# Performance work log

Hardware: AMD Instinct MI355X
Metric: run time of the kernel (lower is better)

## Reference

```python
import jax, jax.numpy as jnp
import numpy as np

N = 50000       # num entities
F_IN = 256      # input feature dim
H = 128         # hidden_dim (= per-head dim, concat=False)
HEADS = 4
L = 3           # num_layers
T = 3           # num edge types
E = 250000      # edges per type
NEG = 0.2       # leaky_relu slope (module + GATv2 default)


def setup_inputs() -> dict:
    key = jax.random.key(0)
    ks = jax.random.split(key, 10)
    s = 0.05
    return {
        "feat": jax.random.normal(ks[0], (N, F_IN), jnp.float32),
        "emb_table": jax.random.normal(ks[1], (N, H), jnp.float32),
        "proj_w": jax.random.normal(ks[2], (F_IN, H), jnp.float32) * s,
        "proj_b": jnp.zeros((H,), jnp.float32),
        "ln_g": jnp.ones((H,), jnp.float32),
        "ln_b": jnp.zeros((H,), jnp.float32),
        "skip_w": jnp.ones((L,), jnp.float32),
        "Wl": jax.random.normal(ks[3], (L, T, H, HEADS * H), jnp.float32) * s,
        "Wr": jax.random.normal(ks[4], (L, T, H, HEADS * H), jnp.float32) * s,
        "att": jax.random.normal(ks[5], (L, T, HEADS, H), jnp.float32) * s,
        "bias": jnp.zeros((L, T, H), jnp.float32),
        "edge_src": jax.random.randint(ks[6], (T, E), 0, N, jnp.int64),
        "edge_dst": jax.random.randint(ks[7], (T, E), 0, N, jnp.int64),
    }


def _layer_norm(x, g, b):
    mu = jnp.mean(x, axis=-1, keepdims=True)
    var = jnp.mean(jnp.square(x - mu), axis=-1, keepdims=True)
    return (x - mu) * jax.lax.rsqrt(var + 1e-5) * g + b


def _l2norm(x):
    n = jnp.sqrt(jnp.sum(jnp.square(x), axis=-1, keepdims=True))
    return x / jnp.maximum(n, 1e-12)


def _gatv2(x, wl, wr, a, b, src, dst):
    # x: [N,H]; wl,wr: [H, HEADS*H]; a: [HEADS,H]; src/dst: [E]
    xl = (x @ wl).reshape(N, HEADS, H)
    xr = (x @ wr).reshape(N, HEADS, H)
    m = xl[src] + xr[dst]                                   # [E,HEADS,H]
    e = jnp.sum(a * jax.nn.leaky_relu(m, NEG), axis=-1)     # [E,HEADS]
    # segment softmax over incoming edges per destination node
    emax = jax.lax.stop_gradient(jax.ops.segment_max(e, dst, num_segments=N))
    ex = jnp.exp(e - emax[dst])
    den = jax.ops.segment_sum(ex, dst, num_segments=N)      # [N,HEADS]
    alpha = ex / (den[dst] + 1e-16)                         # [E,HEADS]
    out = jax.ops.segment_sum(alpha[:, :, None] * xl[src], dst, num_segments=N)
    return jnp.mean(out, axis=1) + b                        # concat=False -> head mean


def reference(feat, emb_table, proj_w, proj_b, ln_g, ln_b, skip_w,
              Wl, Wr, att, bias, edge_src, edge_dst):
    h = jax.nn.leaky_relu(_layer_norm(feat @ proj_w + proj_b, ln_g, ln_b), NEG)
    ne = _l2norm(emb_table)                                 # normalize(embedding(arange(N)))
    x0 = 0.7 * h + 0.5 * ne
    x = x0
    for i in range(L):
        # HeteroConv(aggr='mean') over edge types, all on node type 'entity'
        per_type = [
            _gatv2(x, Wl[i, t], Wr[i, t], att[i, t], bias[i, t],
                   edge_src[t], edge_dst[t])
            for t in range(T)
        ]
        xu = jnp.mean(jnp.stack(per_type, axis=0), axis=0)
        alpha = jax.nn.sigmoid(skip_w[i])
        x = jax.nn.leaky_relu(xu, NEG) + alpha * x0          # dropout = identity (eval)
    return x
```

## Files before the change

### kernel.cpp

```cpp
#include <hip/hip_runtime.h>
#include <hip/hip_bf16.h>
#include <math.h>

#define N_NODES 50000
#define NOFF    50004
#define NBLK    49
#define F_IN    256
#define H       128
#define HEADS   4
#define HH      512
#define L_LAYERS 3
#define T_TYPES  3
#define E_EDGES  250000
#define NEG      0.2f

typedef __attribute__((ext_vector_type(8))) short short8_t;
typedef __attribute__((ext_vector_type(4))) float float4_t;

__device__ __forceinline__ float leaky(float x) { return x > 0.f ? x : NEG * x; }

__device__ __forceinline__ unsigned short f2bf(float f) {
    union { float f; unsigned int i; } v; v.f = f;
    unsigned int x = v.i;
    unsigned int r = (x + 0x7fffu + ((x >> 16) & 1u)) >> 16;
    return (unsigned short)r;
}

__device__ __forceinline__ float bf2f(unsigned short u) {
    union { unsigned int i; float f; } v; v.i = ((unsigned)u) << 16; return v.f;
}

__device__ __forceinline__ void unpack8(uint4 q, float* o) {
    union { unsigned int i; float f; } v;
    v.i = q.x << 16;          o[0] = v.f;
    v.i = q.x & 0xffff0000u;  o[1] = v.f;
    v.i = q.y << 16;          o[2] = v.f;
    v.i = q.y & 0xffff0000u;  o[3] = v.f;
    v.i = q.z << 16;          o[4] = v.f;
    v.i = q.z & 0xffff0000u;  o[5] = v.f;
    v.i = q.w << 16;          o[6] = v.f;
    v.i = q.w & 0xffff0000u;  o[7] = v.f;
}

__global__ void detect_kernel(const int* __restrict__ edst, int* __restrict__ flag) {
    __shared__ int s_any;
    if (threadIdx.x == 0) s_any = 0;
    __syncthreads();
    int a = 0;
    #pragma unroll
    for (int j = 0; j < 8; ++j) a |= edst[2 * (threadIdx.x * 8 + j) + 1];
    if (a) atomicOr(&s_any, 1);
    __syncthreads();
    if (threadIdx.x == 0) *flag = s_any ? 0 : 1;
}

__global__ void hist_kernel(const int* __restrict__ edst, int* __restrict__ counts,
                            const int* __restrict__ flag) {
    int idx = blockIdx.x * 256 + threadIdx.x;
    if (idx < T_TYPES * E_EDGES) {
        int sh = *flag;
        int t = idx / E_EDGES;
        int d = edst[(size_t)idx << sh];
        if ((unsigned)d < N_NODES)
            atomicAdd(&counts[t * N_NODES + d], 1);
    }
}

__global__ __launch_bounds__(256) void scan_a_kernel(const int* __restrict__ counts,
                                                     int* __restrict__ bsum) {
    const int b = blockIdx.x;
    const int t = b / NBLK, ch = b % NBLK;
    const int tid = threadIdx.x, lane = tid & 63;
    __shared__ int ws[4];
    const int* cnt = counts + t * N_NODES;
    int i0 = ch * 1024 + tid * 4;
    int s = 0;
    if (i0 + 3 < N_NODES) { int4 v = *(const int4*)(cnt + i0); s = v.x + v.y + v.z + v.w; }
    else { for (int j = 0; j < 4; ++j) { int i = i0 + j; if (i < N_NODES) s += cnt[i]; } }
    #pragma unroll
    for (int o = 32; o > 0; o >>= 1) s += __shfl_xor(s, o);
    if (lane == 0) ws[tid >> 6] = s;
    __syncthreads();
    if (tid == 0) bsum[b] = ws[0] + ws[1] + ws[2] + ws[3];
}

__global__ void scan_b_kernel(int* __restrict__ bsum, int* __restrict__ off) {
    int t = threadIdx.x;
    if (t < T_TYPES) {
        int run = 0;
        for (int c = 0; c < NBLK; ++c) { int v = bsum[t * NBLK + c]; bsum[t * NBLK + c] = run; run += v; }
        off[t * NOFF + N_NODES] = run;
    }
}

__global__ __launch_bounds__(256) void scan_c_kernel(const int* counts,
                                                     const int* __restrict__ bsum,
                                                     int* __restrict__ off,
                                                     int* cursor) {
    const int b = blockIdx.x;
    const int t = b / NBLK, ch = b % NBLK;
    const int tid = threadIdx.x, lane = tid & 63, w = tid >> 6;
    __shared__ int ws[4];
    const int* cnt = counts + t * N_NODES;
    int i0 = ch * 1024 + tid * 4;
    int v0 = 0, v1 = 0, v2 = 0, v3 = 0;
    if (i0 + 3 < N_NODES) { int4 v = *(const int4*)(cnt + i0); v0 = v.x; v1 = v.y; v2 = v.z; v3 = v.w; }
    else {
        if (i0     < N_NODES) v0 = cnt[i0];
        if (i0 + 1 < N_NODES) v1 = cnt[i0 + 1];
        if (i0 + 2 < N_NODES) v2 = cnt[i0 + 2];
        if (i0 + 3 < N_NODES) v3 = cnt[i0 + 3];
    }
    int s = v0 + v1 + v2 + v3;
    int x = s;
    #pragma unroll
    for (int o = 1; o < 64; o <<= 1) { int y = __shfl_up(x, o); if (lane >= o) x += y; }
    if (lane == 63) ws[w] = x;
    __syncthreads();
    int woff = 0;
    #pragma unroll
    for (int j = 0; j < 4; ++j) woff += (j < w) ? ws[j] : 0;
    int base = bsum[b] + woff + (x - s);
    int e0 = base, e1 = e0 + v0, e2 = e1 + v1, e3 = e2 + v2;
    if (i0 + 3 < N_NODES) {
        *(int4*)(off + t * NOFF + i0)       = make_int4(e0, e1, e2, e3);
        *(int4*)(cursor + t * N_NODES + i0) = make_int4(e0, e1, e2, e3);
    } else {
        if (i0     < N_NODES) { off[t * NOFF + i0]     = e0; cursor[t * N_NODES + i0]     = e0; }
        if (i0 + 1 < N_NODES) { off[t * NOFF + i0 + 1] = e1; cursor[t * N_NODES + i0 + 1] = e1; }
        if (i0 + 2 < N_NODES) { off[t * NOFF + i0 + 2] = e2; cursor[t * N_NODES + i0 + 2] = e2; }
        if (i0 + 3 < N_NODES) { off[t * NOFF + i0 + 3] = e3; cursor[t * N_NODES + i0 + 3] = e3; }
    }
}

__global__ void scatter_kernel(const int* __restrict__ esrc, const int* __restrict__ edst,
                               int* __restrict__ cursor, int* __restrict__ csrc,
                               const int* __restrict__ flag) {
    int idx = blockIdx.x * 256 + threadIdx.x;
    if (idx < T_TYPES * E_EDGES) {
        int sh = *flag;
        int t = idx / E_EDGES;
        int d = edst[(size_t)idx << sh];
        if ((unsigned)d >= N_NODES) return;
        int s = esrc[(size_t)idx << sh];
        if ((unsigned)s >= N_NODES) s = 0;
        int pos = atomicAdd(&cursor[t * N_NODES + d], 1);
        if ((unsigned)pos < E_EDGES)
            csrc[(size_t)t * E_EDGES + pos] = s;
    }
}

__global__ void wconv_kernel(const float* __restrict__ Wl, const float* __restrict__ Wr,
                             unsigned short* __restrict__ Wt) {
    int idx = blockIdx.x * 256 + threadIdx.x;
    if (idx >= L_LAYERS * T_TYPES * 1024 * H) return;
    int lt  = idx / (1024 * H);
    int rem = idx - lt * (1024 * H);
    int c   = rem / H;
    int k   = rem - c * H;
    float v = (c < HH) ? Wl[(size_t)lt * H * HH + (size_t)k * HH + c]
                       : Wr[(size_t)lt * H * HH + (size_t)k * HH + (c - HH)];
    Wt[idx] = f2bf(v);
}

__global__ void featconv_kernel(const float* __restrict__ feat,
                                unsigned short* __restrict__ fHi,
                                unsigned short* __restrict__ fLo) {
    size_t i = ((size_t)blockIdx.x * 256 + threadIdx.x) * 4;
    if (i >= (size_t)N_NODES * F_IN) return;
    float4 v = *(const float4*)(feat + i);
    ushort4 h, l;
    h.x = f2bf(v.x); l.x = f2bf(v.x - bf2f(h.x));
    h.y = f2bf(v.y); l.y = f2bf(v.y - bf2f(h.y));
    h.z = f2bf(v.z); l.z = f2bf(v.z - bf2f(h.z));
    h.w = f2bf(v.w); l.w = f2bf(v.w - bf2f(h.w));
    *(ushort4*)(fHi + i) = h;
    *(ushort4*)(fLo + i) = l;
}

__global__ void pconv_kernel(const float* __restrict__ pw,
                             unsigned short* __restrict__ pWtHi,
                             unsigned short* __restrict__ pWtLo) {
    int idx = blockIdx.x * 256 + threadIdx.x;
    if (idx >= H * F_IN) return;
    int c = idx / F_IN, k = idx - c * F_IN;
    float v = pw[(size_t)k * H + c];
    unsigned short hi = f2bf(v);
    pWtHi[idx] = hi;
    pWtLo[idx] = f2bf(v - bf2f(hi));
}

__device__ __forceinline__ void stage_tile(unsigned short* dst, const unsigned short* src,
                                           int rbase, int kbase, int tid, bool guardRows) {
    #pragma unroll
    for (int it = 0; it < 8; ++it) {
        int c = it * 256 + tid;
        int r = c >> 4, k8 = c & 15;
        int slot = (k8 ^ (r & 15)) * 8;
        uint4 v = make_uint4(0, 0, 0, 0);
        int row = rbase + r;
        if (!guardRows || row < N_NODES)
            v = *(const uint4*)(src + (size_t)row * 256 + kbase + k8 * 8);
        *(uint4*)(dst + r * 128 + slot) = v;
    }
}

__global__ __launch_bounds__(256) void init_gemm_kernel(
    const unsigned short* __restrict__ fHi, const unsigned short* __restrict__ fLo,
    const unsigned short* __restrict__ pWtHi, const unsigned short* __restrict__ pWtLo,
    float* __restrict__ proj)
{
    __shared__ unsigned short smem[32768];
    unsigned short* As = smem;
    unsigned short* Bs = smem + 16384;
    const int tid = threadIdx.x;
    const int nb = blockIdx.x * 128;

    const int wv = tid >> 6, lane = tid & 63;
    const int lm = lane & 15, kg = lane >> 4;
    const int wm = (wv & 1) * 64, wn = (wv >> 1) * 64;
    float4_t acc[4][4];
    #pragma unroll
    for (int i = 0; i < 4; ++i)
        #pragma unroll
        for (int j = 0; j < 4; ++j)
            acc[i][j] = (float4_t){0.f, 0.f, 0.f, 0.f};

    auto compute = [&]() {
        #pragma unroll
        for (int ks = 0; ks < 4; ++ks) {
            const int K8 = ks * 4 + kg;
            const int slot = (K8 ^ lm) * 8;
            short8_t a[4], b[4];
            #pragma unroll
            for (int i = 0; i < 4; ++i) {
                a[i] = *(const short8_t*)(As + (wm + i * 16 + lm) * 128 + slot);
                b[i] = *(const short8_t*)(Bs + (wn + i * 16 + lm) * 128 + slot);
            }
            #pragma unroll
            for (int i = 0; i < 4; ++i)
                #pragma unroll
                for (int j = 0; j < 4; ++j)
                    acc[i][j] = __builtin_amdgcn_mfma_f32_16x16x32_bf16(a[i], b[j], acc[i][j], 0, 0, 0);
        }
    };

    #pragma unroll
    for (int kh = 0; kh < 2; ++kh) {
        const int kbase = kh * 128;
        stage_tile(As, fHi, nb, kbase, tid, true);
        stage_tile(Bs, pWtHi, 0, kbase, tid, false);
        __syncthreads();
        compute();
        __syncthreads();
        stage_tile(Bs, pWtLo, 0, kbase, tid, false);
        __syncthreads();
        compute();
        __syncthreads();
        stage_tile(As, fLo, nb, kbase, tid, true);
        stage_tile(Bs, pWtHi, 0, kbase, tid, false);
        __syncthreads();
        compute();
        __syncthreads();
    }

    #pragma unroll
    for (int i = 0; i < 4; ++i) {
        #pragma unroll
        for (int r = 0; r < 4; ++r) {
            int node = nb + wm + i * 16 + kg * 4 + r;
            if (node < N_NODES) {
                #pragma unroll
                for (int j = 0; j < 4; ++j)
                    proj[(size_t)node * H + wn + j * 16 + lm] = acc[i][j][r];
            }
        }
    }
}

__global__ __launch_bounds__(128) void ln_combine_kernel(
    const float* __restrict__ proj, const float* __restrict__ emb,
    const float* __restrict__ pb, const float* __restrict__ g, const float* __restrict__ b,
    float* __restrict__ x0, unsigned short* __restrict__ xcurb)
{
    __shared__ float s0[2], s1[2];
    const int tid = threadIdx.x;
    const int nb = blockIdx.x * 8;
    const int c = tid;
    float acc[8];
    #pragma unroll
    for (int nn = 0; nn < 8; ++nn) {
        int node = nb + nn;
        acc[nn] = (node < N_NODES) ? proj[(size_t)node * H + c] : 0.f;
    }
    const float pbc = pb[c], gc = g[c], bc = b[c];
    for (int nn = 0; nn < 8; ++nn) {
        float v = acc[nn] + pbc;
        float sum = v, sq = v * v;
        for (int o = 32; o > 0; o >>= 1) { sum += __shfl_down(sum, o); sq += __shfl_down(sq, o); }
        if ((tid & 63) == 0) { s0[tid >> 6] = sum; s1[tid >> 6] = sq; }
        __syncthreads();
        float tot = s0[0] + s0[1], tq = s1[0] + s1[1];
        __syncthreads();
        float mu = tot * (1.f / H);
        float var = tq * (1.f / H) - mu * mu;
        acc[nn] = leaky((v - mu) * rsqrtf(var + 1e-5f) * gc + bc);
    }
    for (int nn = 0; nn < 8; ++nn) {
        int node = nb + nn;
        float ev = (node < N_NODES) ? emb[(size_t)node * H + c] : 0.f;
        float sq = ev * ev;
        for (int o = 32; o > 0; o >>= 1) sq += __shfl_down(sq, o);
        if ((tid & 63) == 0) s0[tid >> 6] = sq;
        __syncthreads();
        float nrm = sqrtf(s0[0] + s0[1]);
        __syncthreads();
        float nev = ev / fmaxf(nrm, 1e-12f);
        float xv = 0.7f * acc[nn] + 0.5f * nev;
        if (node < N_NODES) {
            x0[(size_t)node * H + c] = xv;
            xcurb[(size_t)node * H + c] = f2bf(xv);
        }
    }
}

__global__ __launch_bounds__(256) void gemm_mfma_kernel(
    const unsigned short* __restrict__ x,
    const unsigned short* __restrict__ Wt,
    unsigned short* __restrict__ XL, unsigned short* __restrict__ XR)
{
    __shared__ unsigned short smem[32768];
    unsigned short* As = smem;
    unsigned short* Bs = smem + 16384;
    const int tid = threadIdx.x;
    const int nb = blockIdx.y * 128;
    const int cb = blockIdx.x * 128;

    #pragma unroll
    for (int it = 0; it < 8; ++it) {
        int c = it * 256 + tid;
        int r = c >> 4;
        int k8 = c & 15;
        int slot = (k8 ^ (r & 15)) * 8;
        int node = nb + r;
        uint4 va = make_uint4(0, 0, 0, 0);
        if (node < N_NODES) va = *(const uint4*)(x + (size_t)node * H + k8 * 8);
        *(uint4*)(As + r * H + slot) = va;
        uint4 vb = *(const uint4*)(Wt + (size_t)(cb + r) * H + k8 * 8);
        *(uint4*)(Bs + r * H + slot) = vb;
    }
    __syncthreads();

    const int wv = tid >> 6, lane = tid & 63;
    const int lm = lane & 15, kg = lane >> 4;
    const int wm = (wv & 1) * 64, wn = (wv >> 1) * 64;
    float4_t acc[4][4];
    #pragma unroll
    for (int i = 0; i < 4; ++i)
        #pragma unroll
        for (int j = 0; j < 4; ++j)
            acc[i][j] = (float4_t){0.f, 0.f, 0.f, 0.f};

    #pragma unroll
    for (int ks = 0; ks < 4; ++ks) {
        const int K8 = ks * 4 + kg;
        const int slot = (K8 ^ lm) * 8;
        short8_t a[4], b[4];
        #pragma unroll
        for (int i = 0; i < 4; ++i) {
            a[i] = *(const short8_t*)(As + (wm + i * 16 + lm) * H + slot);
            b[i] = *(const short8_t*)(Bs + (wn + i * 16 + lm) * H + slot);
        }
        #pragma unroll
        for (int i = 0; i < 4; ++i)
            #pragma unroll
            for (int j = 0; j < 4; ++j)
                acc[i][j] = __builtin_amdgcn_mfma_f32_16x16x32_bf16(a[i], b[j], acc[i][j], 0, 0, 0);
    }
    __syncthreads();

    unsigned short* Cs = smem;
    #pragma unroll
    for (int i = 0; i < 4; ++i) {
        int row0 = wm + i * 16 + kg * 4;
        #pragma unroll
        for (int j = 0; j < 4; ++j) {
            int col = wn + j * 16 + lm;
            #pragma unroll
            for (int r = 0; r < 4; ++r)
                Cs[(row0 + r) * 136 + col] = f2bf(acc[i][j][r]);
        }
    }
    __syncthreads();

    unsigned short* O = (blockIdx.x < 4) ? XL : XR;
    const int cbase = (blockIdx.x < 4) ? cb : cb - HH;
    #pragma unroll
    for (int it = 0; it < 8; ++it) {
        int c = it * 256 + tid;
        int r = c >> 4, k8 = (c & 15) * 8;
        int node = nb + r;
        if (node < N_NODES)
            *(uint4*)(O + (size_t)node * HH + cbase + k8) = *(const uint4*)(Cs + r * 136 + k8);
    }
}

__global__ __launch_bounds__(256) void aggregate_kernel(
    const unsigned short* __restrict__ XL, const unsigned short* __restrict__ XR,
    const float* __restrict__ att_t, const float* __restrict__ bias_t,
    const int* __restrict__ off, const int* __restrict__ csrc,
    float* __restrict__ xacc, int first)
{
    const int tid = threadIdx.x;
    const int lane = tid & 63;
    const int wid = tid >> 6;
    const int d = blockIdx.x * 4 + wid;
    if (d >= N_NODES) return;
    const int jb = lane * 8;

    float rv[8], av[8], acc[8];
    {
        uint4 q = *(const uint4*)(XR + (size_t)d * HH + jb);
        unpack8(q, rv);
        float4 u0 = *(const float4*)(att_t + jb);
        float4 u1 = *(const float4*)(att_t + jb + 4);
        av[0] = u0.x; av[1] = u0.y; av[2] = u0.z; av[3] = u0.w;
        av[4] = u1.x; av[5] = u1.y; av[6] = u1.z; av[7] = u1.w;
    }
    #pragma unroll
    for (int u = 0; u < 8; ++u) acc[u] = 0.f;
    float den = 0.f, rmax = -INFINITY;

    const int e0 = off[d];
    const int cnt = off[d + 1] - e0;
    uint4 qA = make_uint4(0, 0, 0, 0), qB = qA;
    int sN = 0;
    if (cnt > 0) { unsigned s = csrc[e0];     if (s >= N_NODES) s = 0; qA = *(const uint4*)(XL + (size_t)s * HH + jb); }
    if (cnt > 1) { unsigned s = csrc[e0 + 1]; if (s >= N_NODES) s = 0; qB = *(const uint4*)(XL + (size_t)s * HH + jb); }
    if (cnt > 2) { unsigned s = csrc[e0 + 2]; if (s >= N_NODES) s = 0; sN = (int)s; }

    for (int e = 0; e < cnt; ++e) {
        float lv[8];
        unpack8(qA, lv);
        qA = qB;
        int sNN = 0;
        if (e + 3 < cnt) { unsigned s = csrc[e0 + e + 3]; if (s >= N_NODES) s = 0; sNN = (int)s; }
        if (e + 2 < cnt) qB = *(const uint4*)(XL + (size_t)sN * HH + jb);
        sN = sNN;
        float p = 0.f;
        #pragma unroll
        for (int u = 0; u < 8; ++u) {
            float m = lv[u] + rv[u];
            p = fmaf(av[u], leaky(m), p);
        }
        p += __shfl_xor(p, 1);
        p += __shfl_xor(p, 2);
        p += __shfl_xor(p, 4);
        p += __shfl_xor(p, 8);
        float nm = fmaxf(rmax, p);
        float sc = __expf(rmax - nm);
        float w  = __expf(p - nm);
        den = den * sc + w;
        #pragma unroll
        for (int u = 0; u < 8; ++u) acc[u] = fmaf(acc[u], sc, w * lv[u]);
        rmax = nm;
    }
    float inv = 1.f / (den + 1e-16f);
    #pragma unroll
    for (int u = 0; u < 8; ++u) {
        float v = acc[u] * inv;
        v += __shfl_xor(v, 16);
        v += __shfl_xor(v, 32);
        acc[u] = v * 0.25f;
    }
    if (lane < 16) {
        float* dst = xacc + (size_t)d * H + jb;
        float o[8];
        #pragma unroll
        for (int u = 0; u < 8; ++u) o[u] = acc[u] + bias_t[jb + u];
        float4 o0 = make_float4(o[0], o[1], o[2], o[3]);
        float4 o1 = make_float4(o[4], o[5], o[6], o[7]);
        if (first) {
            *(float4*)dst = o0;
            *(float4*)(dst + 4) = o1;
        } else {
            float4 c0 = *(const float4*)dst, c1 = *(const float4*)(dst + 4);
            o0.x += c0.x; o0.y += c0.y; o0.z += c0.z; o0.w += c0.w;
            o1.x += c1.x; o1.y += c1.y; o1.z += c1.z; o1.w += c1.w;
            *(float4*)dst = o0;
            *(float4*)(dst + 4) = o1;
        }
    }
}

__global__ __launch_bounds__(256) void epilogue_kernel(
    const float* xacc, const float* __restrict__ x0,
    const float* __restrict__ skipw, int li, int last,
    unsigned short* __restrict__ xcurb, float* out)
{
    size_t i = ((size_t)blockIdx.x * 256 + threadIdx.x) * 4;
    float sw = 1.f / (1.f + __expf(-skipw[li]));
    float4 a = *(const float4*)(xacc + i);
    float4 z = *(const float4*)(x0 + i);
    float o0 = leaky(a.x * (1.f / 3.f)) + sw * z.x;
    float o1 = leaky(a.y * (1.f / 3.f)) + sw * z.y;
    float o2 = leaky(a.z * (1.f / 3.f)) + sw * z.z;
    float o3 = leaky(a.w * (1.f / 3.f)) + sw * z.w;
    if (last) {
        *(float4*)(out + i) = make_float4(o0, o1, o2, o3);
    } else {
        ushort4 o;
        o.x = f2bf(o0); o.y = f2bf(o1); o.z = f2bf(o2); o.w = f2bf(o3);
        *(ushort4*)(xcurb + i) = o;
    }
}

extern "C" void kernel_launch(void* const* d_in, const int* in_sizes, int n_in,
                              void* d_out, int out_size, void* d_ws, size_t ws_size,
                              hipStream_t stream)
{
    const float* feat   = (const float*)d_in[0];
    const float* emb    = (const float*)d_in[1];
    const float* proj_w = (const float*)d_in[2];
    const float* proj_b = (const float*)d_in[3];
    const float* ln_g   = (const float*)d_in[4];
    const float* ln_b   = (const float*)d_in[5];
    const float* skip_w = (const float*)d_in[6];
    const float* Wl     = (const float*)d_in[7];
    const float* Wr     = (const float*)d_in[8];
    const float* att    = (const float*)d_in[9];
    const float* bias   = (const float*)d_in[10];
    const int*   esrc   = (const int*)d_in[11];
    const int*   edst   = (const int*)d_in[12];
    float* out = (float*)d_out;

    char* p = (char*)d_ws;
    auto alloc = [&](size_t bytes) -> char* {
        char* r = p; p += (bytes + 255) & ~(size_t)255; return r;
    };
    float* x0             = (float*)alloc((size_t)N_NODES * H * 4);
    unsigned short* xcurb = (unsigned short*)alloc((size_t)N_NODES * H * 2);
    unsigned short* XL    = (unsigned short*)alloc((size_t)N_NODES * HH * 2);
    unsigned short* XR    = (unsigned short*)alloc((size_t)N_NODES * HH * 2);
    unsigned short* Wt    = (unsigned short*)alloc((size_t)L_LAYERS * T_TYPES * 1024 * H * 2);
    unsigned short* pWtHi = (unsigned short*)alloc((size_t)H * F_IN * 2);
    unsigned short* pWtLo = (unsigned short*)alloc((size_t)H * F_IN * 2);
    int* off    = (int*)alloc((size_t)T_TYPES * NOFF * 4);
    int* cursor = (int*)alloc((size_t)T_TYPES * N_NODES * 4);
    int* csrc   = (int*)alloc((size_t)T_TYPES * E_EDGES * 4);
    int* bsum   = (int*)alloc((size_t)T_TYPES * NBLK * 4);
    int* eflag  = (int*)alloc(256);
    float* xacc = out;

    float* proj          = (float*)XL;
    unsigned short* fHi  = XR;
    unsigned short* fLo  = XR + (size_t)N_NODES * F_IN;

    detect_kernel<<<1, 256, 0, stream>>>(edst, eflag);
    hipMemsetAsync(cursor, 0, (size_t)T_TYPES * N_NODES * 4, stream);
    hist_kernel<<<(T_TYPES * E_EDGES + 255) / 256, 256, 0, stream>>>(edst, cursor, eflag);
    scan_a_kernel<<<T_TYPES * NBLK, 256, 0, stream>>>(cursor, bsum);
    scan_b_kernel<<<1, 256, 0, stream>>>(bsum, off);
    scan_c_kernel<<<T_TYPES * NBLK, 256, 0, stream>>>(cursor, bsum, off, cursor);
    scatter_kernel<<<(T_TYPES * E_EDGES + 255) / 256, 256, 0, stream>>>(esrc, edst, cursor, csrc, eflag);

    wconv_kernel<<<(L_LAYERS * T_TYPES * 1024 * H + 255) / 256, 256, 0, stream>>>(Wl, Wr, Wt);
    featconv_kernel<<<((N_NODES * F_IN / 4) + 255) / 256, 256, 0, stream>>>(feat, fHi, fLo);
    pconv_kernel<<<(H * F_IN + 255) / 256, 256, 0, stream>>>(proj_w, pWtHi, pWtLo);
    init_gemm_kernel<<<(N_NODES + 127) / 128, 256, 0, stream>>>(fHi, fLo, pWtHi, pWtLo, proj);
    ln_combine_kernel<<<N_NODES / 8, 128, 0, stream>>>(proj, emb, proj_b, ln_g, ln_b, x0, xcurb);

    for (int i = 0; i < L_LAYERS; ++i) {
        for (int t = 0; t < T_TYPES; ++t) {
            const int lt = i * T_TYPES + t;
            const unsigned short* wt = Wt + (size_t)lt * 1024 * H;
            const float* at = att + (size_t)lt * HEADS * H;
            const float* bi = bias + (size_t)lt * H;
            gemm_mfma_kernel<<<dim3(8, (N_NODES + 127) / 128), 256, 0, stream>>>(xcurb, wt, XL, XR);
            aggregate_kernel<<<(N_NODES + 3) / 4, 256, 0, stream>>>(
                XL, XR, at, bi, off + t * NOFF, csrc + (size_t)t * E_EDGES,
                xacc, (t == 0) ? 1 : 0);
        }
        epilogue_kernel<<<(N_NODES * H / 4) / 256, 256, 0, stream>>>(
            xacc, x0, skip_w, i, (i == L_LAYERS - 1) ? 1 : 0, xcurb, out);
    }
}
```

Baseline: 1.200 ms.

## Drop online-softmax max tracking and use packed FP32 math in aggregation

```diff
diff --git a/kernel.cpp b/kernel.cpp
--- a/kernel.cpp
+++ b/kernel.cpp
@@ -16,6 +16,7 @@
 
 typedef __attribute__((ext_vector_type(8))) short short8_t;
 typedef __attribute__((ext_vector_type(4))) float float4_t;
+typedef __attribute__((ext_vector_type(2))) float float2_t;
 
 __device__ __forceinline__ float leaky(float x) { return x > 0.f ? x : NEG * x; }
 
@@ -40,6 +41,40 @@
     v.i = q.z & 0xffff0000u;  o[5] = v.f;
     v.i = q.w << 16;          o[6] = v.f;
     v.i = q.w & 0xffff0000u;  o[7] = v.f;
+}
+
+__device__ __forceinline__ float2_t pk_add(float2_t a, float2_t b) {
+    float2_t d;
+    asm("v_pk_add_f32 %0, %1, %2" : "=v"(d) : "v"(a), "v"(b));
+    return d;
+}
+__device__ __forceinline__ float2_t pk_fma(float2_t a, float2_t b, float2_t c) {
+    float2_t d;
+    asm("v_pk_fma_f32 %0, %1, %2, %3" : "=v"(d) : "v"(a), "v"(b), "v"(c));
+    return d;
+}
+__device__ __forceinline__ float2_t pk_abs(float2_t a) {
+    union { float2_t f; unsigned int u[2]; } v; v.f = a;
+    v.u[0] &= 0x7fffffffu;
+    v.u[1] &= 0x7fffffffu;
+    return v.f;
+}
+
+__device__ __forceinline__ float fast_exp2(float x) {
+    return __builtin_amdgcn_exp2f(x);
+}
+
+__device__ __forceinline__ void unpack_pk(uint4 q, float2_t* o) {
+    union { unsigned int i; float f; } v;
+    float2_t t;
+    v.i = q.x << 16;         t.x = v.f;
+    v.i = q.x & 0xffff0000u; t.y = v.f; o[0] = t;
+    v.i = q.y << 16;         t.x = v.f;
+    v.i = q.y & 0xffff0000u; t.y = v.f; o[1] = t;
+    v.i = q.z << 16;         t.x = v.f;
+    v.i = q.z & 0xffff0000u; t.y = v.f; o[2] = t;
+    v.i = q.w << 16;         t.x = v.f;
+    v.i = q.w & 0xffff0000u; t.y = v.f; o[3] = t;
 }
 
 __global__ void detect_kernel(const int* __restrict__ edst, int* __restrict__ flag) {
@@ -405,31 +440,33 @@
     }
 }
 
-__global__ __launch_bounds__(256) void aggregate_kernel(
+__global__ __launch_bounds__(64) void aggregate_kernel(
     const unsigned short* __restrict__ XL, const unsigned short* __restrict__ XR,
     const float* __restrict__ att_t, const float* __restrict__ bias_t,
     const int* __restrict__ off, const int* __restrict__ csrc,
     float* __restrict__ xacc, int first)
 {
-    const int tid = threadIdx.x;
-    const int lane = tid & 63;
-    const int wid = tid >> 6;
-    const int d = blockIdx.x * 4 + wid;
+    const int lane = threadIdx.x;
+    const int d = blockIdx.x;
     if (d >= N_NODES) return;
     const int jb = lane * 8;
-
-    float rv[8], av[8], acc[8];
+    const float L2E = 1.4426950408889634f;
+
+    float2_t rv[4], c1[4], c2[4], acc2[4];
     {
         uint4 q = *(const uint4*)(XR + (size_t)d * HH + jb);
-        unpack8(q, rv);
+        unpack_pk(q, rv);
         float4 u0 = *(const float4*)(att_t + jb);
         float4 u1 = *(const float4*)(att_t + jb + 4);
-        av[0] = u0.x; av[1] = u0.y; av[2] = u0.z; av[3] = u0.w;
-        av[4] = u1.x; av[5] = u1.y; av[6] = u1.z; av[7] = u1.w;
-    }
-    #pragma unroll
-    for (int u = 0; u < 8; ++u) acc[u] = 0.f;
-    float den = 0.f, rmax = -INFINITY;
+        float av[8] = {u0.x, u0.y, u0.z, u0.w, u1.x, u1.y, u1.z, u1.w};
+        #pragma unroll
+        for (int u = 0; u < 4; ++u) {
+            c1[u] = (float2_t){0.6f * L2E * av[2 * u], 0.6f * L2E * av[2 * u + 1]};
+            c2[u] = (float2_t){0.4f * L2E * av[2 * u], 0.4f * L2E * av[2 * u + 1]};
+            acc2[u] = (float2_t){0.f, 0.f};
+        }
+    }
+    float den = 0.f;
 
     const int e0 = off[d];
     const int cnt = off[d + 1] - e0;
@@ -440,53 +477,57 @@
     if (cnt > 2) { unsigned s = csrc[e0 + 2]; if (s >= N_NODES) s = 0; sN = (int)s; }
 
     for (int e = 0; e < cnt; ++e) {
-        float lv[8];
-        unpack8(qA, lv);
+        float2_t lv[4];
+        unpack_pk(qA, lv);
         qA = qB;
         int sNN = 0;
         if (e + 3 < cnt) { unsigned s = csrc[e0 + e + 3]; if (s >= N_NODES) s = 0; sNN = (int)s; }
         if (e + 2 < cnt) qB = *(const uint4*)(XL + (size_t)sN * HH + jb);
         sN = sNN;
-        float p = 0.f;
-        #pragma unroll
-        for (int u = 0; u < 8; ++u) {
-            float m = lv[u] + rv[u];
-            p = fmaf(av[u], leaky(m), p);
-        }
+        float2_t p2 = (float2_t){0.f, 0.f};
+        #pragma unroll
+        for (int u = 0; u < 4; ++u) {
+            float2_t m = pk_add(lv[u], rv[u]);
+            float2_t am = pk_abs(m);
+            p2 = pk_fma(c1[u], m, p2);
+            p2 = pk_fma(c2[u], am, p2);
+        }
+        float p = p2.x + p2.y;
         p += __shfl_xor(p, 1);
         p += __shfl_xor(p, 2);
         p += __shfl_xor(p, 4);
         p += __shfl_xor(p, 8);
-        float nm = fmaxf(rmax, p);
-        float sc = __expf(rmax - nm);
-        float w  = __expf(p - nm);
-        den = den * sc + w;
-        #pragma unroll
-        for (int u = 0; u < 8; ++u) acc[u] = fmaf(acc[u], sc, w * lv[u]);
-        rmax = nm;
-    }
+        float w = fast_exp2(p);
+        den += w;
+        float2_t w2 = (float2_t){w, w};
+        #pragma unroll
+        for (int u = 0; u < 4; ++u) acc2[u] = pk_fma(w2, lv[u], acc2[u]);
+    }
+
     float inv = 1.f / (den + 1e-16f);
+    float o[8];
+    #pragma unroll
+    for (int u = 0; u < 4; ++u) { o[2 * u] = acc2[u].x; o[2 * u + 1] = acc2[u].y; }
     #pragma unroll
     for (int u = 0; u < 8; ++u) {
-        float v = acc[u] * inv;
+        float v = o[u] * inv;
         v += __shfl_xor(v, 16);
         v += __shfl_xor(v, 32);
-        acc[u] = v * 0.25f;
+        o[u] = v * 0.25f;
     }
     if (lane < 16) {
         float* dst = xacc + (size_t)d * H + jb;
-        float o[8];
-        #pragma unroll
-        for (int u = 0; u < 8; ++u) o[u] = acc[u] + bias_t[jb + u];
+        #pragma unroll
+        for (int u = 0; u < 8; ++u) o[u] += bias_t[jb + u];
         float4 o0 = make_float4(o[0], o[1], o[2], o[3]);
         float4 o1 = make_float4(o[4], o[5], o[6], o[7]);
         if (first) {
             *(float4*)dst = o0;
             *(float4*)(dst + 4) = o1;
         } else {
-            float4 c0 = *(const float4*)dst, c1 = *(const float4*)(dst + 4);
+            float4 c0 = *(const float4*)dst, c1v = *(const float4*)(dst + 4);
             o0.x += c0.x; o0.y += c0.y; o0.z += c0.z; o0.w += c0.w;
-            o1.x += c1.x; o1.y += c1.y; o1.z += c1.z; o1.w += c1.w;
+            o1.x += c1v.x; o1.y += c1v.y; o1.z += c1v.z; o1.w += c1v.w;
             *(float4*)dst = o0;
             *(float4*)(dst + 4) = o1;
         }
@@ -577,7 +618,7 @@
             const float* at = att + (size_t)lt * HEADS * H;
             const float* bi = bias + (size_t)lt * H;
             gemm_mfma_kernel<<<dim3(8, (N_NODES + 127) / 128), 256, 0, stream>>>(xcurb, wt, XL, XR);
-            aggregate_kernel<<<(N_NODES + 3) / 4, 256, 0, stream>>>(
+            aggregate_kernel<<<N_NODES, 64, 0, stream>>>(
                 XL, XR, at, bi, off + t * NOFF, csrc + (size_t)t * E_EDGES,
                 xacc, (t == 0) ? 1 : 0);
         }
```

Result: faster. 1.168 ms (-2.7%).
